# Kernel optimization log

Measured on AMD Instinct MI355X. Metric: run time of the kernel, lower is better.

The kernel has to match this reference:

```python
import jax, jax.numpy as jnp
import numpy as np

NUM_HEADS = 8
DIM = 256
SCALE = (DIM // NUM_HEADS) ** -0.5  # head_dim = dim // nhead = 32


def setup_inputs() -> dict:
    key = jax.random.key(0)
    k1, k2, k3, k4, k5 = jax.random.split(key, 5)
    B, N = 1, 4096
    qk = jax.random.normal(k1, (B, N, 3 * DIM), dtype=jnp.float32)
    v_cls = jax.random.normal(k2, (B, N, 2 * DIM), dtype=jnp.float32)
    masks = jax.random.uniform(k3, (B, N, N), dtype=jnp.float32)
    # torch Linear weights stored as [in, out] for x @ W
    W_qk = jax.random.normal(k4, (3 * DIM, 6 * DIM), dtype=jnp.float32) * (3 * DIM) ** -0.5
    W_v = jax.random.normal(k5, (2 * DIM, 2 * DIM), dtype=jnp.float32) * (2 * DIM) ** -0.5
    return {"qk": qk, "v_cls": v_cls, "masks": masks, "W_qk": W_qk, "W_v": W_v}


def reference(qk, v_cls, masks, W_qk, W_v):
    B, N, C_qk = qk.shape
    C_cls = v_cls.shape[-1]
    H = NUM_HEADS
    hd_qk = C_qk // H   # 96
    hd_v = C_cls // H   # 64

    # qk projection: [B,N,6*dim] -> (2,B,H,N,hd_qk)
    proj = (qk @ W_qk).reshape(B, N, 2, H, hd_qk).transpose(2, 0, 3, 1, 4)
    q, k = proj[0], proj[1]                      # [B,H,N,hd_qk]
    v = (v_cls @ W_v).reshape(B, N, H, hd_v).transpose(0, 2, 1, 3)  # [B,H,N,hd_v]

    attn = jnp.einsum('bhnd,bhmd->bhnm', q, k) * SCALE
    attn = jax.nn.softmax(attn, axis=-1)

    # post-softmax mask-mul and renorm by mask-sum and head count
    m = masks[:, None]                           # [B,1,N,N] broadcast over heads
    attn = attn * m / (H * jnp.sum(m, axis=-1, keepdims=True))
    # attn_drop with p=0.0 is identity in eval

    x_cls = jnp.einsum('bhnm,bhmd->bhnd', attn, v)
    return x_cls.transpose(0, 2, 1, 3).reshape(B, N, C_cls)
```

## Files before the change

### kernel.cpp

```cpp
#include <hip/hip_runtime.h>

typedef __attribute__((ext_vector_type(8))) _Float16 half8;
typedef __attribute__((ext_vector_type(4))) _Float16 half4;
typedef __attribute__((ext_vector_type(2))) _Float16 half2;
typedef __attribute__((ext_vector_type(2))) __fp16 fp16x2;
typedef __attribute__((ext_vector_type(4))) float f32x4;

#define N_SEQ 4096
#define HD_QK 96
#define HD_V  64
#define NHEADS 8
#define QSCALE 0.25505545556f
#define ESHIFT 8.0f

union PKC { fp16x2 p; half2 h; };

__device__ inline half2 pk_cvt(float a, float b) {
    PKC u;
    u.p = __builtin_amdgcn_cvt_pkrtz(a, b);
    return u.h;
}

__device__ inline half8 cvt8(float4 a, float4 b) {
    half8 h;
    h[0] = (_Float16)a.x; h[1] = (_Float16)a.y; h[2] = (_Float16)a.z; h[3] = (_Float16)a.w;
    h[4] = (_Float16)b.x; h[5] = (_Float16)b.y; h[6] = (_Float16)b.z; h[7] = (_Float16)b.w;
    return h;
}

__device__ inline void cast_blk(const float* __restrict__ in, _Float16* __restrict__ out,
                                int blk, int t) {
    size_t i = ((size_t)blk * 256 + t) * 8;
    float4 a = *(const float4*)(in + i);
    float4 b = *(const float4*)(in + i + 4);
    *(half8*)(out + i) = cvt8(a, b);
}

__device__ __forceinline__ void gl16(const void* g, void* l) {
    __builtin_amdgcn_global_load_lds(
        (const __attribute__((address_space(1))) unsigned int*)g,
        (__attribute__((address_space(3))) unsigned int*)l, 16, 0, 0);
}

__global__ __launch_bounds__(256) void prep(
    const float* __restrict__ qk, const float* __restrict__ v_cls,
    const float* __restrict__ masks, const float* __restrict__ W_qk,
    const float* __restrict__ W_v,
    _Float16* __restrict__ Xh, _Float16* __restrict__ Vch,
    _Float16* __restrict__ Msw, float* __restrict__ Msum,
    _Float16* __restrict__ Wqkt, _Float16* __restrict__ Wvt)
{
    __shared__ float tile[32][33];
    __shared__ float red[64][17];
    const int bx = blockIdx.x, t = threadIdx.x;
    if (bx < 1536) {
        cast_blk(qk, Xh, bx, t);
    } else if (bx < 2560) {
        cast_blk(v_cls, Vch, bx - 1536, t);
    } else if (bx < 3968) {
        const bool big = bx < 3712;
        const int id = big ? bx - 2560 : bx - 3712;
        const int nx = big ? 48 : 16;
        const int C = big ? 1536 : 512, R = big ? 768 : 512;
        const float* in = big ? W_qk : W_v;
        _Float16* out = big ? Wqkt : Wvt;
        int cx = id % nx, cy = id / nx;
        int tx = t & 31, ty = t >> 5;
        int c0 = cx * 32, r0 = cy * 32;
        for (int k = 0; k < 4; k++)
            tile[ty + 8 * k][tx] = in[(size_t)(r0 + ty + 8 * k) * C + c0 + tx];
        __syncthreads();
        for (int k = 0; k < 4; k++)
            out[(size_t)(c0 + ty + 8 * k) * R + r0 + tx] = (_Float16)tile[tx][ty + 8 * k];
    } else {
        const int id = bx - 3968;
        const int q0b = id >> 6, kb = id & 63;
        const int w = t >> 6, lane = t & 63;
        const int l15 = lane >> 2, quad = lane & 3;
        const int col = kb * 64 + 16 * w + 4 * quad;
        half4 hv[4];
        float ps[4];
        for (int nt = 0; nt < 4; nt++) {
            const float* src = masks + (size_t)(q0b * 64 + 16 * nt + l15) * N_SEQ + col;
            float4 a = *(const float4*)src;
            hv[nt] = half4{(_Float16)a.x, (_Float16)a.y, (_Float16)a.z, (_Float16)a.w};
            ps[nt] = (a.x + a.y) + (a.z + a.w);
        }
        _Float16* dst = Msw + (((size_t)(q0b * 64 + kb) * 4 + w) * 1024) + lane * 16;
        half8 h0, h1;
        for (int j = 0; j < 4; j++) {
            h0[j] = hv[0][j]; h0[4 + j] = hv[1][j];
            h1[j] = hv[2][j]; h1[4 + j] = hv[3][j];
        }
        *(half8*)dst = h0;
        *(half8*)(dst + 8) = h1;
        for (int nt = 0; nt < 4; nt++)
            red[16 * nt + l15][w * 4 + quad] = ps[nt];
        __syncthreads();
        if (t < 64) {
            float s = 0.f;
            for (int i = 0; i < 16; i++) s += red[t][i];
            atomicAdd(&Msum[q0b * 64 + t], s);
        }
    }
}

__global__ __launch_bounds__(256) void proj_fused(
    const _Float16* __restrict__ Xh, const _Float16* __restrict__ Vch,
    const _Float16* __restrict__ Wqkt, const _Float16* __restrict__ Wvt,
    _Float16* __restrict__ Qh, _Float16* __restrict__ Kh,
    _Float16* __restrict__ Vtg)
{
    __shared__ _Float16 smem[192 * 72];
    _Float16 (*Xs)[72] = (_Float16 (*)[72])smem;
    _Float16 (*Ws)[72] = (_Float16 (*)[72])(smem + 128 * 72);

    const int t = threadIdx.x;
    const int lane = t & 63, wv = t >> 6;
    const int quad = lane >> 4, l15 = lane & 15;
    const bool qkmode = blockIdx.x < 24;
    const int n0 = qkmode ? blockIdx.x * 64 : (blockIdx.x - 24) * 64;
    const int row0 = blockIdx.y * 128;
    const int K = qkmode ? 768 : 512;
    const _Float16* X = qkmode ? Xh : Vch;
    const _Float16* Wt = qkmode ? Wqkt : Wvt;

    const int mB = (wv & 1) * 64, nB = (wv >> 1) * 32;
    const int sr = t >> 1, sk = (t & 1) * 32;
    const int sr2 = t >> 2, sk2 = (t & 3) * 16;

    const f32x4 fzero = {0.f, 0.f, 0.f, 0.f};
    f32x4 acc[4][2];
    for (int i = 0; i < 4; i++)
        for (int j = 0; j < 2; j++) acc[i][j] = fzero;

    for (int k0 = 0; k0 < K; k0 += 64) {
        __syncthreads();
        {
            const _Float16* xp = X + (size_t)(row0 + sr) * K + k0 + sk;
            *(half8*)&Xs[sr][sk]      = *(const half8*)xp;
            *(half8*)&Xs[sr][sk + 8]  = *(const half8*)(xp + 8);
            *(half8*)&Xs[sr][sk + 16] = *(const half8*)(xp + 16);
            *(half8*)&Xs[sr][sk + 24] = *(const half8*)(xp + 24);
            const _Float16* wp = Wt + (size_t)(n0 + sr2) * K + k0 + sk2;
            *(half8*)&Ws[sr2][sk2]     = *(const half8*)wp;
            *(half8*)&Ws[sr2][sk2 + 8] = *(const half8*)(wp + 8);
        }
        __syncthreads();
        for (int c = 0; c < 2; c++) {
            half8 af[4], bf[2];
            for (int i = 0; i < 4; i++)
                af[i] = *(const half8*)&Xs[mB + 16 * i + l15][c * 32 + quad * 8];
            for (int j = 0; j < 2; j++)
                bf[j] = *(const half8*)&Ws[nB + 16 * j + l15][c * 32 + quad * 8];
            for (int i = 0; i < 4; i++)
                for (int j = 0; j < 2; j++)
                    acc[i][j] = __builtin_amdgcn_mfma_f32_16x16x32_f16(af[i], bf[j], acc[i][j], 0, 0, 0);
        }
    }

    __syncthreads();
    _Float16 (*Ct)[72] = (_Float16 (*)[72])smem;
    for (int j = 0; j < 2; j++) {
        int col = n0 + nB + 16 * j + l15;
        float scl = (qkmode && col < 768) ? QSCALE : 1.0f;
        for (int i = 0; i < 4; i++)
            for (int r = 0; r < 4; r++)
                Ct[mB + 16 * i + quad * 4 + r][nB + 16 * j + l15] =
                    (_Float16)(acc[i][j][r] * scl);
    }
    __syncthreads();

    if (qkmode) {
        for (int e = 0; e < 4; e++) {
            int id = e * 256 + t;
            int row = id >> 3, cc = id & 7;
            int col = n0 + cc * 8;
            int w = col >= 768 ? 1 : 0;
            int rem = col - w * 768;
            int h = rem / 96, d = rem - h * 96;
            _Float16* dst = w ? Kh : Qh;
            *(half8*)&dst[((size_t)h * N_SEQ + row0 + row) * HD_QK + d] =
                *(const half8*)&Ct[row][cc * 8];
        }
    } else {
        for (int e = 0; e < 2; e++) {
            int id = e * 256 + t;
            int col = id >> 3, rc = id & 7;
            int c = n0 + col;
            int h = c >> 6, d = c & 63;
            half8 v0, v1;
            for (int k = 0; k < 8; k++) {
                v0[k] = Ct[rc * 16 + k][col];
                v1[k] = Ct[rc * 16 + 8 + k][col];
            }
            _Float16* dst = &Vtg[((size_t)h * HD_V + d) * N_SEQ + row0 + rc * 16];
            *(half8*)dst = v0;
            *(half8*)(dst + 8) = v1;
        }
    }
}

__global__ __launch_bounds__(256, 3) void flash_attn(
    const _Float16* __restrict__ Qh, const _Float16* __restrict__ Kh,
    const _Float16* __restrict__ Vtg, const _Float16* __restrict__ Msw,
    _Float16* __restrict__ Owsh, float* __restrict__ Lws)
{
    __shared__ __align__(16) char smem[40960];

    const int t = threadIdx.x;
    const int lane = t & 63, w = t >> 6;
    const int quad = lane >> 4, l15 = lane & 15;
    const int bx = blockIdx.x;
    const int q0b = bx & 63;
    const int hz = bx >> 6;
    const int head = hz & 7;
    const int z = hz >> 3;
    const int q0 = q0b * 64;
    const int kb0 = 21 * z, kbE = (z == 2) ? 64 : kb0 + 21;

    half8 qf[3][4];
    for (int nt = 0; nt < 4; nt++) {
        const _Float16* qp = Qh + ((size_t)head * N_SEQ + q0 + 16 * nt + l15) * HD_QK + 8 * quad;
        for (int c = 0; c < 3; c++)
            qf[c][nt] = *(const half8*)(qp + 32 * c);
    }

    const char* kgb = (const char*)Kh
        + ((size_t)(head * N_SEQ + 16 * w + l15) * HD_QK + 8 * quad) * 2;
    const char* vgb = (const char*)Vtg
        + ((size_t)(head * HD_V + lane) * N_SEQ) * 2 + 32 * w;
    const _Float16* mbase = Msw + ((size_t)(q0b * 64 + kb0) * 4 + w) * 1024
                                + (l15 * 4 + quad) * 16;

    char* stW = smem + w * 10240;

    const f32x4 fzero = {0.f, 0.f, 0.f, 0.f};
    const f32x4 minit = {-ESHIFT, -ESHIFT, -ESHIFT, -ESHIFT};
    f32x4 oacc[4][4];
    for (int nt = 0; nt < 4; nt++)
        for (int v = 0; v < 4; v++) oacc[nt][v] = fzero;
    float lsum[4] = {0.f, 0.f, 0.f, 0.f};

    half8 m01, m23;

    {
        char* kd = stW;
        const char* ks = kgb + (size_t)kb0 * 12288;
        gl16(ks, kd);
        gl16(ks + 64, kd + 1024);
        gl16(ks + 128, kd + 2048);
        char* vd = stW + 3072;
        const char* vs = vgb + (size_t)kb0 * 128;
        gl16(vs, vd);
        gl16(vs + 16, vd + 1024);
    }
    m01 = *(const half8*)mbase;
    m23 = *(const half8*)(mbase + 8);

    int cur = 0;
    for (int j = kb0; j < kbE; j++, cur ^= 1) {
        asm volatile("s_waitcnt vmcnt(2)" ::: "memory");
        __builtin_amdgcn_sched_barrier(0);

        const char* kl = stW + cur * 5120;
        half8 kf[3];
        kf[0] = *(const half8*)(kl + lane * 16);
        kf[1] = *(const half8*)(kl + 1024 + lane * 16);
        kf[2] = *(const half8*)(kl + 2048 + lane * 16);
        const char* vl = kl + 3072 + (quad >> 1) * 1024 + l15 * 16 + (quad & 1) * 8;
        half4 vf[4];
        vf[0] = *(const half4*)(vl);
        vf[1] = *(const half4*)(vl + 256);
        vf[2] = *(const half4*)(vl + 512);
        vf[3] = *(const half4*)(vl + 768);

        const int jn = j + 1;
        {
            char* kd = stW + (cur ^ 1) * 5120;
            const char* ks = kgb + (size_t)jn * 12288;
            gl16(ks, kd);
            gl16(ks + 64, kd + 1024);
            gl16(ks + 128, kd + 2048);
            char* vd = kd + 3072;
            const char* vs = vgb + (size_t)jn * 128;
            gl16(vs, vd);
            gl16(vs + 16, vd + 1024);
        }

        f32x4 sT[4];
        for (int nt = 0; nt < 4; nt++) {
            f32x4 s = __builtin_amdgcn_mfma_f32_16x16x32_f16(kf[0], qf[0][nt], minit, 0, 0, 0);
            s = __builtin_amdgcn_mfma_f32_16x16x32_f16(kf[1], qf[1][nt], s, 0, 0, 0);
            s = __builtin_amdgcn_mfma_f32_16x16x32_f16(kf[2], qf[2][nt], s, 0, 0, 0);
            sT[nt] = s;
        }

        half4 af[4];
        {
            half2 mh[8];
            for (int i = 0; i < 4; i++) {
                mh[i]     = half2{m01[2 * i], m01[2 * i + 1]};
                mh[4 + i] = half2{m23[2 * i], m23[2 * i + 1]};
            }
            for (int nt = 0; nt < 4; nt++) {
                float p0 = __builtin_amdgcn_exp2f(sT[nt][0]);
                float p1 = __builtin_amdgcn_exp2f(sT[nt][1]);
                float p2 = __builtin_amdgcn_exp2f(sT[nt][2]);
                float p3 = __builtin_amdgcn_exp2f(sT[nt][3]);
                lsum[nt] += (p0 + p1) + (p2 + p3);
                half2 lo = pk_cvt(p0, p1) * mh[2 * nt];
                half2 hi = pk_cvt(p2, p3) * mh[2 * nt + 1];
                af[nt] = half4{lo[0], lo[1], hi[0], hi[1]};
            }
        }
        {
            const _Float16* mp = mbase + (size_t)(jn - kb0) * 4096;
            m01 = *(const half8*)mp;
            m23 = *(const half8*)(mp + 8);
        }

        for (int nt = 0; nt < 4; nt++)
            for (int v = 0; v < 4; v++)
                oacc[nt][v] = __builtin_amdgcn_mfma_f32_16x16x16f16(af[nt], vf[v], oacc[nt][v], 0, 0, 0);
    }

    __syncthreads();

    float (*Ob)[64][68] = (float (*)[64][68])smem;
    float (*Lb)[64] = (float (*)[64])(smem + 34816);

    for (int nt = 0; nt < 4; nt++) {
        lsum[nt] += __shfl_xor(lsum[nt], 16);
        lsum[nt] += __shfl_xor(lsum[nt], 32);
    }

    if (w & 1) {
        for (int nt = 0; nt < 4; nt++) {
            for (int v = 0; v < 4; v++)
                for (int r = 0; r < 4; r++)
                    Ob[w >> 1][16 * nt + 4 * quad + r][16 * v + l15] = oacc[nt][v][r];
            if (quad == 0) Lb[w >> 1][16 * nt + l15] = lsum[nt];
        }
    }
    __syncthreads();
    if (!(w & 1)) {
        for (int nt = 0; nt < 4; nt++) {
            for (int v = 0; v < 4; v++)
                for (int r = 0; r < 4; r++)
                    Ob[w >> 1][16 * nt + 4 * quad + r][16 * v + l15] += oacc[nt][v][r];
            if (quad == 0) Lb[w >> 1][16 * nt + l15] += lsum[nt];
        }
    }
    __syncthreads();

    {
        int row = t >> 2, c0 = (t & 3) * 16;
        _Float16* obase = Owsh + (size_t)z * N_SEQ * 512 + (size_t)(q0 + row) * 512
                          + head * HD_V + c0;
        for (int g = 0; g < 2; g++) {
            half8 h;
            for (int j2 = 0; j2 < 8; j2++)
                h[j2] = (_Float16)(Ob[0][row][c0 + 8 * g + j2] + Ob[1][row][c0 + 8 * g + j2]);
            *(half8*)(obase + 8 * g) = h;
        }
        if (t < 64)
            Lws[((size_t)z * NHEADS + head) * N_SEQ + q0 + t] = Lb[0][t] + Lb[1][t];
    }
}

__global__ __launch_bounds__(256) void finalize(
    const _Float16* __restrict__ Owsh, const float* __restrict__ Lws,
    const float* __restrict__ Msum, float* __restrict__ out)
{
    const size_t ZSTR = (size_t)N_SEQ * 512;
    size_t o = ((size_t)blockIdx.x * 256 + threadIdx.x) * 8;
    int q = (int)(o >> 9);
    int head = (int)((o & 511) >> 6);
    half8 p0 = *(const half8*)(Owsh + o);
    half8 p1 = *(const half8*)(Owsh + ZSTR + o);
    half8 p2 = *(const half8*)(Owsh + 2 * ZSTR + o);
    float l = Lws[(size_t)head * N_SEQ + q]
            + Lws[((size_t)NHEADS + head) * N_SEQ + q]
            + Lws[((size_t)2 * NHEADS + head) * N_SEQ + q];
    float inv = 1.0f / (l * (float)NHEADS * Msum[q]);
    float4 r0, r1;
    r0.x = ((float)p0[0] + (float)p1[0] + (float)p2[0]) * inv;
    r0.y = ((float)p0[1] + (float)p1[1] + (float)p2[1]) * inv;
    r0.z = ((float)p0[2] + (float)p1[2] + (float)p2[2]) * inv;
    r0.w = ((float)p0[3] + (float)p1[3] + (float)p2[3]) * inv;
    r1.x = ((float)p0[4] + (float)p1[4] + (float)p2[4]) * inv;
    r1.y = ((float)p0[5] + (float)p1[5] + (float)p2[5]) * inv;
    r1.z = ((float)p0[6] + (float)p1[6] + (float)p2[6]) * inv;
    r1.w = ((float)p0[7] + (float)p1[7] + (float)p2[7]) * inv;
    *(float4*)(out + o) = r0;
    *(float4*)(out + o + 4) = r1;
}

extern "C" void kernel_launch(void* const* d_in, const int* in_sizes, int n_in,
                              void* d_out, int out_size, void* d_ws, size_t ws_size,
                              hipStream_t stream) {
    const float* qk    = (const float*)d_in[0];
    const float* v_cls = (const float*)d_in[1];
    const float* masks = (const float*)d_in[2];
    const float* W_qk  = (const float*)d_in[3];
    const float* W_v   = (const float*)d_in[4];
    float* out = (float*)d_out;

    char* wsp = (char*)d_ws;
    _Float16* Xh   = (_Float16*)(wsp);
    _Float16* Vch  = (_Float16*)(wsp + (size_t)6291456);
    _Float16* Wqkt = (_Float16*)(wsp + (size_t)10485760);
    _Float16* Wvt  = (_Float16*)(wsp + (size_t)12845056);
    _Float16* Owsh = (_Float16*)(wsp);
    size_t off = 13631488;
    auto allocB = [&](size_t bytes) { char* p = wsp + off; off += (bytes + 255) & ~(size_t)255; return p; };
    _Float16* Qh   = (_Float16*)allocB((size_t)NHEADS * N_SEQ * HD_QK * 2);
    _Float16* Kh   = (_Float16*)allocB((size_t)NHEADS * N_SEQ * HD_QK * 2);
    _Float16* Vtg  = (_Float16*)allocB((size_t)NHEADS * HD_V * N_SEQ * 2);
    _Float16* Msw  = (_Float16*)allocB((size_t)N_SEQ * N_SEQ * 2);
    float*    Msum = (float*)allocB((size_t)N_SEQ * 4);
    float*    Lws  = (float*)allocB((size_t)3 * NHEADS * N_SEQ * 4);
    (void)allocB((size_t)16384);
    (void)ws_size;

    dim3 blk(256);
    (void)hipMemsetAsync(Msum, 0, N_SEQ * sizeof(float), stream);
    prep<<<dim3(8064), blk, 0, stream>>>(
        qk, v_cls, masks, W_qk, W_v, Xh, Vch, Msw, Msum, Wqkt, Wvt);

    proj_fused<<<dim3(32, N_SEQ / 128), blk, 0, stream>>>(
        Xh, Vch, Wqkt, Wvt, Qh, Kh, Vtg);

    flash_attn<<<dim3(1536), blk, 0, stream>>>(
        Qh, Kh, Vtg, Msw, Owsh, Lws);

    finalize<<<dim3((N_SEQ * 512) / (256 * 8)), blk, 0, stream>>>(
        Owsh, Lws, Msum, out);
}
```

Baseline: 250.7 us.

## Triple-buffer K tiles to prefetch two iterations ahead in flash attention

Splits the per-wave LDS staging into a three-slot K ring and a separate two-slot V buffer, so K tiles are fetched two iterations ahead while V and the mask stay one ahead. Issue order is pinned with sched_barriers and the wait count becomes vmcnt(3). The goal is to hide more global-load latency behind the QK MFMAs. In exchange LDS per block grows from 40 KB to 52 KB, which may lower occupancy below the 3-blocks launch bound. The final iteration prefetches K past the block range, and the workspace padding is enlarged to cover that out-of-range read.

After: 314.7 us. 1.26x slower.

```diff
diff --git a/kernel.cpp b/kernel.cpp
--- a/kernel.cpp
+++ b/kernel.cpp
@@ -206,7 +206,7 @@
     const _Float16* __restrict__ Vtg, const _Float16* __restrict__ Msw,
     _Float16* __restrict__ Owsh, float* __restrict__ Lws)
 {
-    __shared__ __align__(16) char smem[40960];
+    __shared__ __align__(16) char smem[53248];
 
     const int t = threadIdx.x;
     const int lane = t & 63, w = t >> 6;
@@ -233,7 +233,8 @@
     const _Float16* mbase = Msw + ((size_t)(q0b * 64 + kb0) * 4 + w) * 1024
                                 + (l15 * 4 + quad) * 16;
 
-    char* stW = smem + w * 10240;
+    char* stW = smem + w * 13312;
+    char* stV = stW + 9216;
 
     const f32x4 fzero = {0.f, 0.f, 0.f, 0.f};
     const f32x4 minit = {-ESHIFT, -ESHIFT, -ESHIFT, -ESHIFT};
@@ -245,48 +246,75 @@
     half8 m01, m23;
 
     {
-        char* kd = stW;
         const char* ks = kgb + (size_t)kb0 * 12288;
-        gl16(ks, kd);
-        gl16(ks + 64, kd + 1024);
-        gl16(ks + 128, kd + 2048);
-        char* vd = stW + 3072;
+        gl16(ks, stW);
+        gl16(ks + 64, stW + 1024);
+        gl16(ks + 128, stW + 2048);
+    }
+    __builtin_amdgcn_sched_barrier(0);
+    {
         const char* vs = vgb + (size_t)kb0 * 128;
-        gl16(vs, vd);
-        gl16(vs + 16, vd + 1024);
-    }
+        gl16(vs, stV);
+        gl16(vs + 16, stV + 1024);
+    }
+    __builtin_amdgcn_sched_barrier(0);
     m01 = *(const half8*)mbase;
     m23 = *(const half8*)(mbase + 8);
-
+    __builtin_amdgcn_sched_barrier(0);
+    {
+        const char* ks = kgb + (size_t)(kb0 + 1) * 12288;
+        gl16(ks, stW + 3072);
+        gl16(ks + 64, stW + 3072 + 1024);
+        gl16(ks + 128, stW + 3072 + 2048);
+    }
+    __builtin_amdgcn_sched_barrier(0);
+
+    int ksl = 0;
     int cur = 0;
-    for (int j = kb0; j < kbE; j++, cur ^= 1) {
-        asm volatile("s_waitcnt vmcnt(2)" ::: "memory");
+    for (int j = kb0; j < kbE; j++) {
+        asm volatile("s_waitcnt vmcnt(3)" ::: "memory");
         __builtin_amdgcn_sched_barrier(0);
 
-        const char* kl = stW + cur * 5120;
+        const char* kl = stW + ksl * 3072;
         half8 kf[3];
         kf[0] = *(const half8*)(kl + lane * 16);
         kf[1] = *(const half8*)(kl + 1024 + lane * 16);
         kf[2] = *(const half8*)(kl + 2048 + lane * 16);
-        const char* vl = kl + 3072 + (quad >> 1) * 1024 + l15 * 16 + (quad & 1) * 8;
+        const char* vl = stV + cur * 2048 + (quad >> 1) * 1024 + l15 * 16 + (quad & 1) * 8;
         half4 vf[4];
         vf[0] = *(const half4*)(vl);
         vf[1] = *(const half4*)(vl + 256);
         vf[2] = *(const half4*)(vl + 512);
         vf[3] = *(const half4*)(vl + 768);
 
-        const int jn = j + 1;
+        half2 mh[8];
+        for (int i = 0; i < 4; i++) {
+            mh[i]     = half2{m01[2 * i], m01[2 * i + 1]};
+            mh[4 + i] = half2{m23[2 * i], m23[2 * i + 1]};
+        }
+        __builtin_amdgcn_sched_barrier(0);
+
         {
-            char* kd = stW + (cur ^ 1) * 5120;
-            const char* ks = kgb + (size_t)jn * 12288;
+            const char* vs = vgb + (size_t)(j + 1) * 128;
+            char* vd = stV + (cur ^ 1) * 2048;
+            gl16(vs, vd);
+            gl16(vs + 16, vd + 1024);
+        }
+        __builtin_amdgcn_sched_barrier(0);
+        {
+            const _Float16* mp = mbase + (size_t)(j + 1 - kb0) * 4096;
+            m01 = *(const half8*)mp;
+            m23 = *(const half8*)(mp + 8);
+        }
+        __builtin_amdgcn_sched_barrier(0);
+        {
+            const char* ks = kgb + (size_t)(j + 2) * 12288;
+            char* kd = stW + ((ksl + 2) % 3) * 3072;
             gl16(ks, kd);
             gl16(ks + 64, kd + 1024);
             gl16(ks + 128, kd + 2048);
-            char* vd = kd + 3072;
-            const char* vs = vgb + (size_t)jn * 128;
-            gl16(vs, vd);
-            gl16(vs + 16, vd + 1024);
-        }
+        }
+        __builtin_amdgcn_sched_barrier(0);
 
         f32x4 sT[4];
         for (int nt = 0; nt < 4; nt++) {
@@ -297,32 +325,23 @@
         }
 
         half4 af[4];
-        {
-            half2 mh[8];
-            for (int i = 0; i < 4; i++) {
-                mh[i]     = half2{m01[2 * i], m01[2 * i + 1]};
-                mh[4 + i] = half2{m23[2 * i], m23[2 * i + 1]};
-            }
-            for (int nt = 0; nt < 4; nt++) {
-                float p0 = __builtin_amdgcn_exp2f(sT[nt][0]);
-                float p1 = __builtin_amdgcn_exp2f(sT[nt][1]);
-                float p2 = __builtin_amdgcn_exp2f(sT[nt][2]);
-                float p3 = __builtin_amdgcn_exp2f(sT[nt][3]);
-                lsum[nt] += (p0 + p1) + (p2 + p3);
-                half2 lo = pk_cvt(p0, p1) * mh[2 * nt];
-                half2 hi = pk_cvt(p2, p3) * mh[2 * nt + 1];
-                af[nt] = half4{lo[0], lo[1], hi[0], hi[1]};
-            }
-        }
-        {
-            const _Float16* mp = mbase + (size_t)(jn - kb0) * 4096;
-            m01 = *(const half8*)mp;
-            m23 = *(const half8*)(mp + 8);
+        for (int nt = 0; nt < 4; nt++) {
+            float p0 = __builtin_amdgcn_exp2f(sT[nt][0]);
+            float p1 = __builtin_amdgcn_exp2f(sT[nt][1]);
+            float p2 = __builtin_amdgcn_exp2f(sT[nt][2]);
+            float p3 = __builtin_amdgcn_exp2f(sT[nt][3]);
+            lsum[nt] += (p0 + p1) + (p2 + p3);
+            half2 lo = pk_cvt(p0, p1) * mh[2 * nt];
+            half2 hi = pk_cvt(p2, p3) * mh[2 * nt + 1];
+            af[nt] = half4{lo[0], lo[1], hi[0], hi[1]};
         }
 
         for (int nt = 0; nt < 4; nt++)
             for (int v = 0; v < 4; v++)
                 oacc[nt][v] = __builtin_amdgcn_mfma_f32_16x16x16f16(af[nt], vf[v], oacc[nt][v], 0, 0, 0);
+
+        ksl = (ksl + 1) == 3 ? 0 : ksl + 1;
+        cur ^= 1;
     }
 
     __syncthreads();
@@ -421,7 +440,7 @@
     _Float16* Msw  = (_Float16*)allocB((size_t)N_SEQ * N_SEQ * 2);
     float*    Msum = (float*)allocB((size_t)N_SEQ * 4);
     float*    Lws  = (float*)allocB((size_t)3 * NHEADS * N_SEQ * 4);
-    (void)allocB((size_t)16384);
+    (void)allocB((size_t)131072);
     (void)ws_size;
 
     dim3 blk(256);
```
